# Kernel tuning notes

Hardware: AMD Instinct MI355X
Metric: run time of the kernel (lower is better)

The kernel has to match this reference:

```python
import jax, jax.numpy as jnp
import numpy as np

B, LT, D, N, H = 16, 512, 1024, 4096, 16
LN_EPS = 1e-5


def setup_inputs() -> dict:
    key = jax.random.key(0)
    ks = jax.random.split(key, 10)
    s = 0.02
    struct_token = jax.random.normal(ks[0], (N, D), dtype=jnp.float32)
    text_token = jax.random.normal(ks[1], (B, LT, D), dtype=jnp.float32)
    # contiguous, sorted segment ids: 256 struct tokens per batch element
    struct_batch = jnp.repeat(jnp.arange(B, dtype=jnp.int32), N // B)
    return {
        "struct_token": struct_token,
        "text_token": text_token,
        "in_proj_w": jax.random.normal(ks[2], (3 * D, D), dtype=jnp.float32) * s,
        "in_proj_b": jnp.zeros((3 * D,), jnp.float32),
        "attn_out_w": jax.random.normal(ks[3], (D, D), dtype=jnp.float32) * s,
        "attn_out_b": jnp.zeros((D,), jnp.float32),
        "ln_g": jnp.ones((D,), jnp.float32),
        "ln_b": jnp.zeros((D,), jnp.float32),
        "proj_w": jax.random.normal(ks[4], (D, D), dtype=jnp.float32) * s,
        "proj_b": jnp.zeros((D,), jnp.float32),
        "struct_batch": struct_batch,
        "L_max": N // B,
    }


def reference(struct_token, text_token, in_proj_w, in_proj_b, attn_out_w,
              attn_out_b, ln_g, ln_b, proj_w, proj_b, struct_batch, L_max):
    Bq = text_token.shape[0]
    Dm = struct_token.shape[-1]
    dh = Dm // H
    Ntok = struct_token.shape[0]

    # ---- ragged pad-pack (struct_batch is sorted/contiguous per segment) ----
    counts = jnp.bincount(struct_batch, length=Bq)                 # [B]
    starts = jnp.concatenate([jnp.zeros((1,), counts.dtype),
                              jnp.cumsum(counts)[:-1]])            # [B]
    pos = jnp.arange(Ntok) - starts[struct_batch]                  # [N] position in segment
    padded = jnp.zeros((Bq, L_max, Dm), struct_token.dtype)
    padded = padded.at[struct_batch, pos].set(struct_token)        # [B, Ls, D]

    # ---- nn.MultiheadAttention (batch_first): Q=padded, K=V=text ----
    wq, wk, wv = in_proj_w[:Dm], in_proj_w[Dm:2 * Dm], in_proj_w[2 * Dm:]
    bq, bk, bv = in_proj_b[:Dm], in_proj_b[Dm:2 * Dm], in_proj_b[2 * Dm:]
    q = (padded @ wq.T + bq).reshape(Bq, L_max, H, dh)
    k = (text_token @ wk.T + bk).reshape(Bq, -1, H, dh)
    v = (text_token @ wv.T + bv).reshape(Bq, -1, H, dh)
    scores = jnp.einsum('bqhd,bkhd->bhqk', q, k) / jnp.sqrt(jnp.float32(dh))
    attn = jax.nn.softmax(scores, axis=-1)
    ctx = jnp.einsum('bhqk,bkhd->bqhd', attn, v).reshape(Bq, L_max, Dm)
    fused = ctx @ attn_out_w.T + attn_out_b                        # [B, Ls, D]

    # ---- LayerNorm + output projection ----
    mu = fused.mean(-1, keepdims=True)
    var = fused.var(-1, keepdims=True)
    fused = (fused - mu) * jax.lax.rsqrt(var + LN_EPS) * ln_g + ln_b
    fused = fused @ proj_w.T + proj_b

    # ---- unpack valid tokens + scatter-mean over segments ----
    tok = fused[struct_batch, pos]                                 # [N, D]
    seg_sum = jax.ops.segment_sum(tok, struct_batch, num_segments=Bq)
    return seg_sum / jnp.maximum(counts, 1)[:, None].astype(seg_sum.dtype)
```

## Files before the change

kernel.cpp:

```cpp
#include <hip/hip_runtime.h>

constexpr int B  = 16;
constexpr int LT = 512;
constexpr int D  = 1024;
constexpr int N  = 4096;
constexpr int H  = 16;
constexpr int DH = D / H;
constexpr int LMAX = N / B;
constexpr float LN_EPS = 1e-5f;

typedef short  s16x8 __attribute__((ext_vector_type(8)));
typedef float  f32x4 __attribute__((ext_vector_type(4)));

__device__ __forceinline__ unsigned short f2bf(float x) {
    unsigned int u = __float_as_uint(x);
    unsigned int r = (u + 0x7fffu + ((u >> 16) & 1u)) >> 16;
    return (unsigned short)r;
}
__device__ __forceinline__ float bf2f(unsigned short u) {
    return __uint_as_float((unsigned int)u << 16);
}

__device__ __forceinline__ void load_lds16(const void* g, void* l) {
    __builtin_amdgcn_global_load_lds(
        (const __attribute__((address_space(1))) unsigned int*)g,
        (__attribute__((address_space(3))) unsigned int*)l, 16, 0, 0);
}

__global__ void prep_kernel(const int* __restrict__ sb, int* __restrict__ counts,
                            int* __restrict__ starts, int* __restrict__ pos) {
    __shared__ int s_counts[B], s_starts[B];
    int t = threadIdx.x;
    if (t < B) s_counts[t] = 0;
    __syncthreads();
    for (int i = t; i < N; i += 256) atomicAdd(&s_counts[sb[i]], 1);
    __syncthreads();
    if (t == 0) {
        int run = 0;
        for (int b = 0; b < B; b++) { s_starts[b] = run; run += s_counts[b]; }
    }
    __syncthreads();
    if (t < B) { counts[t] = s_counts[t]; starts[t] = s_starts[t]; }
    for (int i = t; i < N; i += 256) {
        int b = sb[i];
        pos[i] = i - s_starts[b];
    }
}

__global__ void scatter_kernel(const float* __restrict__ st, const int* __restrict__ sb,
                               const int* __restrict__ pos, unsigned short* __restrict__ padded) {
    int i = blockIdx.x;
    int b = sb[i], p = pos[i];
    int d = threadIdx.x * 4;
    float4 v = *(const float4*)&st[(size_t)i * D + d];
    ushort4 o;
    o.x = f2bf(v.x); o.y = f2bf(v.y); o.z = f2bf(v.z); o.w = f2bf(v.w);
    *(ushort4*)&padded[((size_t)(b * LMAX + p)) * D + d] = o;
}

__global__ __launch_bounds__(256) void cast3_kernel(
        const float* __restrict__ x0, unsigned short* __restrict__ y0, int n0,
        const float* __restrict__ x1, unsigned short* __restrict__ y1, int n1,
        const float* __restrict__ x2, unsigned short* __restrict__ y2, int n2) {
    long long i = (long long)(blockIdx.x * 256 + threadIdx.x) * 8;
    const float* x; unsigned short* y;
    if (i < n0)                { x = x0 + i; y = y0 + i; }
    else if (i < (long long)n0 + n1) { long long j = i - n0; x = x1 + j; y = y1 + j; }
    else if (i < (long long)n0 + n1 + n2) { long long j = i - n0 - n1; x = x2 + j; y = y2 + j; }
    else return;
    float4 a = *(const float4*)x;
    float4 b = *(const float4*)(x + 4);
    ushort4 o1, o2;
    o1.x = f2bf(a.x); o1.y = f2bf(a.y); o1.z = f2bf(a.z); o1.w = f2bf(a.w);
    o2.x = f2bf(b.x); o2.y = f2bf(b.y); o2.z = f2bf(b.z); o2.w = f2bf(b.w);
    *(ushort4*)y = o1;
    *(ushort4*)(y + 4) = o2;
}

constexpr int PANEL = 128 * 32;

template<typename Epi>
__device__ __forceinline__ void gemm_tile_e(const unsigned short* __restrict__ A,
                                            const unsigned short* __restrict__ W,
                                            int K, int m0, int n0,
                                            unsigned short* As, unsigned short* Bs,
                                            Epi&& epi) {
    const int tid  = threadIdx.x;
    const int lane = tid & 63;
    const int wave = tid >> 6;
    const int wm = (wave >> 1) * 64, wn = (wave & 1) * 64;

    const int srow = tid >> 2;
    const int scol = (tid & 3) * 8;
    const unsigned short* Ag = A + (size_t)(m0 + srow) * K + scol;
    const unsigned short* Wg = W + (size_t)(n0 + srow) * K + scol;
    unsigned short* Asl = As + tid * 8;
    unsigned short* Bsl = Bs + tid * 8;

    const int fm = lane & 15;
    const int fk = (lane >> 4) * 8;

    f32x4 acc[4][4];
#pragma unroll
    for (int i = 0; i < 4; i++)
#pragma unroll
        for (int j = 0; j < 4; j++) acc[i][j] = (f32x4){0.f, 0.f, 0.f, 0.f};

    for (int k0 = 0; k0 < K; k0 += 64) {
        __syncthreads();
        load_lds16(Ag + k0, Asl);
        load_lds16(Ag + (size_t)64 * K + k0, Asl + 64 * 32);
        load_lds16(Wg + k0, Bsl);
        load_lds16(Wg + (size_t)64 * K + k0, Bsl + 64 * 32);
        load_lds16(Ag + k0 + 32, Asl + PANEL);
        load_lds16(Ag + (size_t)64 * K + k0 + 32, Asl + PANEL + 64 * 32);
        load_lds16(Wg + k0 + 32, Bsl + PANEL);
        load_lds16(Wg + (size_t)64 * K + k0 + 32, Bsl + PANEL + 64 * 32);
        __syncthreads();

#pragma unroll
        for (int hp = 0; hp < 2; hp++) {
            const unsigned short* Ap = As + hp * PANEL;
            const unsigned short* Bp = Bs + hp * PANEL;
            s16x8 af[4], bf[4];
#pragma unroll
            for (int i = 0; i < 4; i++) {
                af[i] = *(const s16x8*)&Ap[(wm + i * 16 + fm) * 32 + fk];
                bf[i] = *(const s16x8*)&Bp[(wn + i * 16 + fm) * 32 + fk];
            }
#pragma unroll
            for (int i = 0; i < 4; i++)
#pragma unroll
                for (int j = 0; j < 4; j++)
                    acc[i][j] = __builtin_amdgcn_mfma_f32_16x16x32_bf16(af[i], bf[j], acc[i][j], 0, 0, 0);
        }
    }

    const int fr = (lane >> 4) * 4;
#pragma unroll
    for (int j = 0; j < 4; j++) {
        int col = n0 + wn + j * 16 + fm;
#pragma unroll
        for (int i = 0; i < 4; i++) {
            int row = m0 + wm + i * 16 + fr;
#pragma unroll
            for (int r = 0; r < 4; r++)
                epi(row + r, col, acc[i][j][r]);
        }
    }
}

__global__ __launch_bounds__(256) void qkv_fused(const unsigned short* __restrict__ padded,
                                                 const unsigned short* __restrict__ text,
                                                 const unsigned short* __restrict__ wqkv,
                                                 const float* __restrict__ bqkv,
                                                 unsigned short* __restrict__ qpack,
                                                 unsigned short* __restrict__ kpack,
                                                 unsigned short* __restrict__ vpack) {
    __shared__ __align__(16) unsigned short As[2 * PANEL];
    __shared__ __align__(16) unsigned short Bs[2 * PANEL];
    int flat = blockIdx.x;
    if (flat < 256) {
        gemm_tile_e(padded, wqkv, D, (flat >> 3) * 128, (flat & 7) * 128, As, Bs,
            [&](int m, int col, float v) {
                float val = v + bqkv[col];
                int b = m >> 8, q = m & 255;
                int h = col >> 6, d = col & 63;
                qpack[(size_t)(b * H + h) * 16384 + (d >> 3) * 2048 + q * 8 + (d & 7)] = f2bf(val);
            });
    } else if (flat < 768) {
        int f = flat - 256;
        gemm_tile_e(text, wqkv + (size_t)D * D, D, (f >> 3) * 128, (f & 7) * 128, As, Bs,
            [&](int m, int col, float v) {
                float val = v + bqkv[D + col];
                int b = m >> 9, key = m & 511;
                int h = col >> 6, d = col & 63;
                kpack[(size_t)(b * H + h) * 32768 + (d >> 3) * 4096 + key * 8 + (d & 7)] = f2bf(val);
            });
    } else {
        int f = flat - 768;
        gemm_tile_e(wqkv + 2 * (size_t)D * D, text, D, (f >> 6) * 128, (f & 63) * 128, As, Bs,
            [&](int m, int col, float v) {
                float val = v + bqkv[2 * D + m];
                int h = m >> 6, d = m & 63;
                int b = col >> 9, key = col & 511;
                vpack[(size_t)(b * H + h) * 32768 + (key >> 3) * 512 + d * 8 + (key & 7)] = f2bf(val);
            });
    }
}

__global__ __launch_bounds__(256) void gemm_bf(const unsigned short* __restrict__ A,
                                               const unsigned short* __restrict__ W,
                                               const float* __restrict__ bias,
                                               unsigned short* __restrict__ C, int Nn, int K) {
    __shared__ __align__(16) unsigned short As[2 * PANEL];
    __shared__ __align__(16) unsigned short Bs[2 * PANEL];
    gemm_tile_e(A, W, K, blockIdx.y * 128, blockIdx.x * 128, As, Bs,
        [&](int m, int col, float v) {
            C[(size_t)m * Nn + col] = f2bf(v + bias[col]);
        });
}

__global__ __launch_bounds__(256) void attn_mfma(const unsigned short* __restrict__ qpack,
                                                 const unsigned short* __restrict__ kpack,
                                                 const unsigned short* __restrict__ vpack,
                                                 unsigned short* __restrict__ ctx) {
    __shared__ __align__(16) unsigned short Ps[4 * 16 * 136];

    const int tid = threadIdx.x;
    const int lane = tid & 63;
    const int wv = tid >> 6;
    const int fm = lane & 15;
    const int quad = lane >> 4;
    const int b = blockIdx.z, h = blockIdx.y;
    const int q0 = blockIdx.x * 64 + wv * 16;

    const unsigned short* qp = qpack + (size_t)(b * H + h) * 16384;
    const unsigned short* kp = kpack + (size_t)(b * H + h) * 32768;
    const unsigned short* vp = vpack + (size_t)(b * H + h) * 32768;

    const s16x8 aq0 = *(const s16x8*)&qp[(quad)     * 2048 + (q0 + fm) * 8];
    const s16x8 aq1 = *(const s16x8*)&qp[(4 + quad) * 2048 + (q0 + fm) * 8];

    f32x4 sc[32];
#pragma unroll
    for (int t = 0; t < 32; t++) {
        s16x8 bk0 = *(const s16x8*)&kp[(quad)     * 4096 + (t * 16 + fm) * 8];
        s16x8 bk1 = *(const s16x8*)&kp[(4 + quad) * 4096 + (t * 16 + fm) * 8];
        f32x4 a = (f32x4){0.f, 0.f, 0.f, 0.f};
        a = __builtin_amdgcn_mfma_f32_16x16x32_bf16(aq0, bk0, a, 0, 0, 0);
        a = __builtin_amdgcn_mfma_f32_16x16x32_bf16(aq1, bk1, a, 0, 0, 0);
        sc[t] = a;
    }

    const float scale = 0.125f;
    float mx[4], l[4], inv[4];
#pragma unroll
    for (int r = 0; r < 4; r++) {
        float m = sc[0][r];
#pragma unroll
        for (int t = 1; t < 32; t++) m = fmaxf(m, sc[t][r]);
        mx[r] = m;
    }
#pragma unroll
    for (int o = 1; o < 16; o <<= 1)
#pragma unroll
        for (int r = 0; r < 4; r++) mx[r] = fmaxf(mx[r], __shfl_xor(mx[r], o));
#pragma unroll
    for (int r = 0; r < 4; r++) l[r] = 0.f;
#pragma unroll
    for (int t = 0; t < 32; t++)
#pragma unroll
        for (int r = 0; r < 4; r++) {
            float e = __expf((sc[t][r] - mx[r]) * scale);
            sc[t][r] = e;
            l[r] += e;
        }
#pragma unroll
    for (int o = 1; o < 16; o <<= 1)
#pragma unroll
        for (int r = 0; r < 4; r++) l[r] += __shfl_xor(l[r], o);
#pragma unroll
    for (int r = 0; r < 4; r++) inv[r] = 1.f / l[r];

    f32x4 co[4];
#pragma unroll
    for (int n = 0; n < 4; n++) co[n] = (f32x4){0.f, 0.f, 0.f, 0.f};
    unsigned short* Pw = Ps + wv * (16 * 136);

    for (int c = 0; c < 4; c++) {
#pragma unroll
        for (int t = 0; t < 8; t++)
#pragma unroll
            for (int r = 0; r < 4; r++)
                Pw[(quad * 4 + r) * 136 + t * 16 + fm] = f2bf(sc[c * 8 + t][r]);
#pragma unroll
        for (int s = 0; s < 4; s++) {
            s16x8 ap = *(const s16x8*)&Pw[fm * 136 + s * 32 + quad * 8];
#pragma unroll
            for (int n = 0; n < 4; n++) {
                s16x8 bv = *(const s16x8*)&vp[(c * 16 + s * 4 + quad) * 512 + (n * 16 + fm) * 8];
                co[n] = __builtin_amdgcn_mfma_f32_16x16x32_bf16(ap, bv, co[n], 0, 0, 0);
            }
        }
    }

    const size_t obase = (size_t)(b * LMAX + q0) * D + h * DH;
#pragma unroll
    for (int n = 0; n < 4; n++)
#pragma unroll
        for (int r = 0; r < 4; r++)
            ctx[obase + (size_t)(quad * 4 + r) * D + n * 16 + fm] = f2bf(co[n][r] * inv[r]);
}

__global__ __launch_bounds__(256) void lnmean_kernel(const unsigned short* __restrict__ f1,
                                                     const float* __restrict__ g,
                                                     const float* __restrict__ bb,
                                                     const int* __restrict__ counts,
                                                     float* __restrict__ msum) {
    int b = blockIdx.x;
    int cnt = counts[b];
    int s0 = blockIdx.y * 32;
    int s1 = min(cnt, s0 + 32);
    if (s0 >= s1) return;
    int t = threadIdx.x;
    int wv = t >> 6, ln = t & 63;
    float4 gg = ((const float4*)g)[t];
    float4 bv = ((const float4*)bb)[t];
    float acc[4] = {0.f, 0.f, 0.f, 0.f};
    __shared__ float red[8];

    for (int s = s0; s < s1; s++) {
        const unsigned short* x = f1 + ((size_t)(b * LMAX + s)) * D;
        ushort4 u = ((const ushort4*)x)[t];
        float4 val = {bf2f(u.x), bf2f(u.y), bf2f(u.z), bf2f(u.w)};
        float sm = val.x + val.y + val.z + val.w;
        float ss = val.x * val.x + val.y * val.y + val.z * val.z + val.w * val.w;
#pragma unroll
        for (int o = 32; o; o >>= 1) { sm += __shfl_xor(sm, o); ss += __shfl_xor(ss, o); }
        if (ln == 0) { red[wv] = sm; red[4 + wv] = ss; }
        __syncthreads();
        sm = red[0] + red[1] + red[2] + red[3];
        ss = red[4] + red[5] + red[6] + red[7];
        __syncthreads();
        float mu = sm * (1.f / D);
        float var = ss * (1.f / D) - mu * mu;
        float r = rsqrtf(var + LN_EPS);
        acc[0] += (val.x - mu) * r * gg.x + bv.x;
        acc[1] += (val.y - mu) * r * gg.y + bv.y;
        acc[2] += (val.z - mu) * r * gg.z + bv.z;
        acc[3] += (val.w - mu) * r * gg.w + bv.w;
    }
    float inv = 1.f / (float)max(cnt, 1);
#pragma unroll
    for (int j = 0; j < 4; j++)
        atomicAdd(&msum[(size_t)b * D + t * 4 + j], acc[j] * inv);
}

__global__ __launch_bounds__(256) void tproj_kernel(const float* __restrict__ msum,
                                                    const float* __restrict__ W,
                                                    const float* __restrict__ bias,
                                                    float* __restrict__ out) {
    int lane = threadIdx.x & 63;
    int n = blockIdx.x * 4 + (threadIdx.x >> 6);
    float4 wr[4];
#pragma unroll
    for (int i = 0; i < 4; i++)
        wr[i] = *(const float4*)&W[(size_t)n * D + i * 256 + lane * 4];
    float bn = bias[n];
    for (int b = 0; b < B; b++) {
        float s = 0.f;
#pragma unroll
        for (int i = 0; i < 4; i++) {
            float4 m4 = *(const float4*)&msum[(size_t)b * D + i * 256 + lane * 4];
            s += m4.x * wr[i].x + m4.y * wr[i].y + m4.z * wr[i].z + m4.w * wr[i].w;
        }
#pragma unroll
        for (int o = 32; o; o >>= 1) s += __shfl_xor(s, o);
        if (lane == 0) out[(size_t)b * D + n] = s + bn;
    }
}

extern "C" void kernel_launch(void* const* d_in, const int* in_sizes, int n_in,
                              void* d_out, int out_size, void* d_ws, size_t ws_size,
                              hipStream_t stream) {
    const float* struct_token = (const float*)d_in[0];
    const float* text_token   = (const float*)d_in[1];
    const float* in_proj_w    = (const float*)d_in[2];
    const float* in_proj_b    = (const float*)d_in[3];
    const float* attn_out_w   = (const float*)d_in[4];
    const float* attn_out_b   = (const float*)d_in[5];
    const float* ln_g         = (const float*)d_in[6];
    const float* ln_b         = (const float*)d_in[7];
    const float* proj_w       = (const float*)d_in[8];
    const float* proj_b       = (const float*)d_in[9];
    const int*   sb           = (const int*)d_in[10];
    float* out = (float*)d_out;

    const size_t MQ  = (size_t)B * LMAX;
    const size_t MKV = (size_t)B * LT;

    char* p = (char*)d_ws;
    unsigned short* padded_b = (unsigned short*)p;  p += MQ * D * 2;
    unsigned short* text_b   = (unsigned short*)p;  p += MKV * D * 2;
    unsigned short* wqkv_b   = (unsigned short*)p;  p += (size_t)3 * D * D * 2;
    unsigned short* wattn_b  = (unsigned short*)p;  p += (size_t)D * D * 2;
    unsigned short* qpack    = (unsigned short*)p;  p += MQ * D * 2;
    unsigned short* kpack    = (unsigned short*)p;  p += MKV * D * 2;
    unsigned short* vpack    = (unsigned short*)p;  p += MKV * D * 2;
    unsigned short* ctx_b    = (unsigned short*)p;  p += MQ * D * 2;
    unsigned short* f1b      = (unsigned short*)p;  p += MQ * D * 2;
    float* msum = (float*)p;  p += (size_t)B * D * 4;
    int* pos    = (int*)p;  p += N * 4;
    int* counts = (int*)p;  p += B * 4;
    int* starts = (int*)p;  p += B * 4;

    hipMemsetAsync(padded_b, 0, MQ * D * 2, stream);
    hipMemsetAsync(msum, 0, (size_t)B * D * 4, stream);
    prep_kernel<<<1, 256, 0, stream>>>(sb, counts, starts, pos);
    scatter_kernel<<<N, 256, 0, stream>>>(struct_token, sb, pos, padded_b);

    cast3_kernel<<<6144, 256, 0, stream>>>(
        text_token, text_b, (int)(MKV * D),
        in_proj_w,  wqkv_b, 3 * D * D,
        attn_out_w, wattn_b, D * D);

    qkv_fused<<<1280, 256, 0, stream>>>(padded_b, text_b, wqkv_b, in_proj_b,
                                        qpack, kpack, vpack);

    attn_mfma<<<dim3(LMAX / 64, H, B), 256, 0, stream>>>(qpack, kpack, vpack, ctx_b);

    gemm_bf<<<dim3(D / 128, MQ / 128), 256, 0, stream>>>(ctx_b, wattn_b, attn_out_b, f1b, D, D);

    lnmean_kernel<<<dim3(B, LMAX / 32), 256, 0, stream>>>(f1b, ln_g, ln_b, counts, msum);

    tproj_kernel<<<256, 256, 0, stream>>>(msum, proj_w, proj_b, out);
}
```

Measured before the change: 307.4 us.

## Stage K/V tiles in LDS and double block size in attention kernel

```diff
diff --git a/kernel.cpp b/kernel.cpp
--- a/kernel.cpp
+++ b/kernel.cpp
@@ -201,36 +201,49 @@
         });
 }
 
-__global__ __launch_bounds__(256) void attn_mfma(const unsigned short* __restrict__ qpack,
+constexpr int PKW = 72;
+
+__global__ __launch_bounds__(512) void attn_mfma(const unsigned short* __restrict__ qpack,
                                                  const unsigned short* __restrict__ kpack,
                                                  const unsigned short* __restrict__ vpack,
                                                  unsigned short* __restrict__ ctx) {
-    __shared__ __align__(16) unsigned short Ps[4 * 16 * 136];
+    __shared__ __align__(16) unsigned short KV[16384];
+    __shared__ __align__(16) unsigned short Ps[8 * 16 * PKW];
 
     const int tid = threadIdx.x;
     const int lane = tid & 63;
     const int wv = tid >> 6;
     const int fm = lane & 15;
     const int quad = lane >> 4;
-    const int b = blockIdx.z, h = blockIdx.y;
-    const int q0 = blockIdx.x * 64 + wv * 16;
+    const int h = blockIdx.x, b = blockIdx.y, half = blockIdx.z;
+    const int q0 = half * 128 + wv * 16;
 
     const unsigned short* qp = qpack + (size_t)(b * H + h) * 16384;
     const unsigned short* kp = kpack + (size_t)(b * H + h) * 32768;
     const unsigned short* vp = vpack + (size_t)(b * H + h) * 32768;
 
-    const s16x8 aq0 = *(const s16x8*)&qp[(quad)     * 2048 + (q0 + fm) * 8];
+    const s16x8 aq0 = *(const s16x8*)&qp[quad * 2048 + (q0 + fm) * 8];
     const s16x8 aq1 = *(const s16x8*)&qp[(4 + quad) * 2048 + (q0 + fm) * 8];
 
     f32x4 sc[32];
-#pragma unroll
-    for (int t = 0; t < 32; t++) {
-        s16x8 bk0 = *(const s16x8*)&kp[(quad)     * 4096 + (t * 16 + fm) * 8];
-        s16x8 bk1 = *(const s16x8*)&kp[(4 + quad) * 4096 + (t * 16 + fm) * 8];
-        f32x4 a = (f32x4){0.f, 0.f, 0.f, 0.f};
-        a = __builtin_amdgcn_mfma_f32_16x16x32_bf16(aq0, bk0, a, 0, 0, 0);
-        a = __builtin_amdgcn_mfma_f32_16x16x32_bf16(aq1, bk1, a, 0, 0, 0);
-        sc[t] = a;
+
+    for (int kc = 0; kc < 2; kc++) {
+        __syncthreads();
+#pragma unroll
+        for (int it = 0; it < 4; it++) {
+            int f = it * 512 + tid;
+            load_lds16(kp + (f >> 8) * 4096 + kc * 2048 + (f & 255) * 8, KV + f * 8);
+        }
+        __syncthreads();
+#pragma unroll
+        for (int t = 0; t < 16; t++) {
+            s16x8 bk0 = *(const s16x8*)&KV[quad * 2048 + (t * 16 + fm) * 8];
+            s16x8 bk1 = *(const s16x8*)&KV[(4 + quad) * 2048 + (t * 16 + fm) * 8];
+            f32x4 a = (f32x4){0.f, 0.f, 0.f, 0.f};
+            a = __builtin_amdgcn_mfma_f32_16x16x32_bf16(aq0, bk0, a, 0, 0, 0);
+            a = __builtin_amdgcn_mfma_f32_16x16x32_bf16(aq1, bk1, a, 0, 0, 0);
+            sc[kc * 16 + t] = a;
+        }
     }
 
     const float scale = 0.125f;
@@ -266,21 +279,31 @@
     f32x4 co[4];
 #pragma unroll
     for (int n = 0; n < 4; n++) co[n] = (f32x4){0.f, 0.f, 0.f, 0.f};
-    unsigned short* Pw = Ps + wv * (16 * 136);
-
-    for (int c = 0; c < 4; c++) {
-#pragma unroll
-        for (int t = 0; t < 8; t++)
-#pragma unroll
-            for (int r = 0; r < 4; r++)
-                Pw[(quad * 4 + r) * 136 + t * 16 + fm] = f2bf(sc[c * 8 + t][r]);
-#pragma unroll
-        for (int s = 0; s < 4; s++) {
-            s16x8 ap = *(const s16x8*)&Pw[fm * 136 + s * 32 + quad * 8];
-#pragma unroll
-            for (int n = 0; n < 4; n++) {
-                s16x8 bv = *(const s16x8*)&vp[(c * 16 + s * 4 + quad) * 512 + (n * 16 + fm) * 8];
-                co[n] = __builtin_amdgcn_mfma_f32_16x16x32_bf16(ap, bv, co[n], 0, 0, 0);
+    unsigned short* Pw = Ps + wv * (16 * PKW);
+
+    for (int vc = 0; vc < 2; vc++) {
+        __syncthreads();
+#pragma unroll
+        for (int it = 0; it < 4; it++) {
+            int f = it * 512 + tid;
+            load_lds16(vp + vc * 16384 + f * 8, KV + f * 8);
+        }
+        __syncthreads();
+        for (int cs = 0; cs < 4; cs++) {
+            int c = vc * 4 + cs;
+#pragma unroll
+            for (int tt = 0; tt < 4; tt++)
+#pragma unroll
+                for (int r = 0; r < 4; r++)
+                    Pw[(quad * 4 + r) * PKW + tt * 16 + fm] = f2bf(sc[c * 4 + tt][r]);
+#pragma unroll
+            for (int s = 0; s < 2; s++) {
+                s16x8 ap = *(const s16x8*)&Pw[fm * PKW + s * 32 + quad * 8];
+#pragma unroll
+                for (int n = 0; n < 4; n++) {
+                    s16x8 bv = *(const s16x8*)&KV[(cs * 8 + s * 4 + quad) * 512 + (n * 16 + fm) * 8];
+                    co[n] = __builtin_amdgcn_mfma_f32_16x16x32_bf16(ap, bv, co[n], 0, 0, 0);
+                }
             }
         }
     }
@@ -408,7 +431,7 @@
     qkv_fused<<<1280, 256, 0, stream>>>(padded_b, text_b, wqkv_b, in_proj_b,
                                         qpack, kpack, vpack);
 
-    attn_mfma<<<dim3(LMAX / 64, H, B), 256, 0, stream>>>(qpack, kpack, vpack, ctx_b);
+    attn_mfma<<<dim3(H, B, 2), 512, 0, stream>>>(qpack, kpack, vpack, ctx_b);
 
     gemm_bf<<<dim3(D / 128, MQ / 128), 256, 0, stream>>>(ctx_b, wattn_b, attn_out_b, f1b, D, D);
 
```

Result: faster. 286.7 us (-6.7%).
